# Kernel optimization log

Measured on AMD Instinct MI355X. Metric: run time of the kernel, lower is better.

The kernel has to match this reference:

```python
import jax, jax.numpy as jnp
import numpy as np

B, T, D = 4, 2048, 2048
H = 16
NOPE, ROPE, VD = 64, 64, 128
QK = NOPE + ROPE  # 128
KV_R, Q_R = 512, 1024
EPS = 1e-6
THETA = 10000.0
SCALE = 1.0 / np.sqrt(QK)


def rmsnorm(x, g):
    var = jnp.mean(jnp.square(x), axis=-1, keepdims=True)
    return x * jax.lax.rsqrt(var + EPS) * g


def rope_tables(seq_len, dim):
    inv_freq = 1.0 / (THETA ** (np.arange(0, dim, 2, dtype=np.float32) / dim))
    t = np.arange(seq_len, dtype=np.float32)
    freqs = np.outer(t, inv_freq)              # [T, dim/2]
    emb = np.concatenate([freqs, freqs], -1)   # [T, dim]
    return jnp.asarray(np.cos(emb)), jnp.asarray(np.sin(emb))


def rotate_half(x):
    x1, x2 = jnp.split(x, 2, axis=-1)
    return jnp.concatenate([-x2, x1], axis=-1)


def apply_rope(x, cos, sin):
    # x: [B,H,S,dim]; cos/sin: [S,dim] -> broadcast over B,H
    return x * cos[None, None] + rotate_half(x) * sin[None, None]


def setup_inputs() -> dict:
    key = jax.random.key(0)
    ks = jax.random.split(key, 10)
    w = lambda k, shp: jax.random.normal(k, shp, jnp.float32) * 0.02
    return {
        'x': jax.random.normal(ks[0], (B, T, D), jnp.float32),
        'w_q_down': w(ks[1], (D, Q_R)),
        'g_q_down': jnp.ones((Q_R,), jnp.float32),
        'w_q_up': w(ks[2], (Q_R, H * QK)),
        'w_kv_down': w(ks[3], (D, KV_R)),
        'g_kv_down': jnp.ones((KV_R,), jnp.float32),
        'w_k_up': w(ks[4], (KV_R, H * NOPE)),
        'w_v_up': w(ks[5], (KV_R, H * VD)),
        'w_k_rope': w(ks[6], (D, ROPE)),
        'g_q': jnp.ones((QK,), jnp.float32),
        'g_k': jnp.ones((QK,), jnp.float32),
        'w_gate': w(ks[7], (D, H * VD)),
        'w_o': w(ks[8], (H * VD, D)),
    }


def reference(x, w_q_down, g_q_down, w_q_up, w_kv_down, g_kv_down,
              w_k_up, w_v_up, w_k_rope, g_q, g_k, w_gate, w_o):
    cos, sin = rope_tables(T, ROPE)

    # Low-rank Q: down-proj -> RMSNorm -> up-proj
    q_c = rmsnorm(x @ w_q_down, g_q_down)                       # [B,T,Q_R]
    q = (q_c @ w_q_up).reshape(B, T, H, QK).transpose(0, 2, 1, 3)  # [B,H,T,QK]
    q_nope, q_rope = q[..., :NOPE], q[..., NOPE:]

    # Low-rank KV compression
    c_kv = rmsnorm(x @ w_kv_down, g_kv_down)                    # [B,S,KV_R]
    k_rope = x @ w_k_rope                                       # [B,S,ROPE]
    S = T
    k_nope = (c_kv @ w_k_up).reshape(B, S, H, NOPE).transpose(0, 2, 1, 3)
    v = (c_kv @ w_v_up).reshape(B, S, H, VD).transpose(0, 2, 1, 3)

    # Decoupled RoPE: shared k_rope broadcast over heads
    k_rope = jnp.broadcast_to(k_rope[:, None], (B, H, S, ROPE))
    q_rope = apply_rope(q_rope, cos[:T], sin[:T])
    k_rope = apply_rope(k_rope, cos[:S], sin[:S])

    q = rmsnorm(jnp.concatenate([q_nope, q_rope], -1), g_q)     # [B,H,T,QK]
    k = rmsnorm(jnp.concatenate([k_nope, k_rope], -1), g_k)     # [B,H,S,QK]

    # Causal SDPA
    scores = jnp.einsum('bhtd,bhsd->bhts', q, k) * SCALE
    mask = jnp.tril(jnp.ones((T, S), bool))
    scores = jnp.where(mask, scores, jnp.finfo(scores.dtype).min)
    attn = jax.nn.softmax(scores, axis=-1)
    out = jnp.einsum('bhts,bhsd->bhtd', attn, v)                # [B,H,T,VD]

    # Gating
    gate = (x @ w_gate).reshape(B, T, H, VD).transpose(0, 2, 1, 3)
    out = out * jax.nn.silu(gate)

    out = out.transpose(0, 2, 1, 3).reshape(B, T, H * VD)
    return out @ w_o
```

## Files before the change

kernel.cpp:

```cpp
#include <hip/hip_runtime.h>
#include <hip/hip_bf16.h>
#include <math.h>

typedef __bf16 bf16_t;
typedef __bf16 bf16x8 __attribute__((ext_vector_type(8)));
typedef float f32x4 __attribute__((ext_vector_type(4)));

#define SCALE_F 0.08838834764831845f
#define SMAX_F 14.0f

#define GLOAD_LDS16(gp, lp)                                              \
    __builtin_amdgcn_global_load_lds(                                    \
        (const __attribute__((address_space(1))) void*)(gp),             \
        (__attribute__((address_space(3))) void*)(lp), 16, 0, 0)

__global__ void k_convert(const float* __restrict__ in, bf16_t* __restrict__ out, int n) {
    int i = (blockIdx.x * 256 + threadIdx.x) * 4;
    if (i >= n) return;
    float4 f = *(const float4*)(in + i);
    out[i + 0] = (bf16_t)f.x;
    out[i + 1] = (bf16_t)f.y;
    out[i + 2] = (bf16_t)f.z;
    out[i + 3] = (bf16_t)f.w;
}

__global__ void k_transpose(const float* __restrict__ w, bf16_t* __restrict__ wt, int K, int N) {
    __shared__ float tile[32][33];
    int n0 = blockIdx.x * 32, k0 = blockIdx.y * 32;
    int tx = threadIdx.x & 31, ty = threadIdx.x >> 5;
#pragma unroll
    for (int i = 0; i < 32; i += 8)
        tile[ty + i][tx] = w[(size_t)(k0 + ty + i) * N + (n0 + tx)];
    __syncthreads();
#pragma unroll
    for (int i = 0; i < 32; i += 8)
        wt[(size_t)(n0 + ty + i) * K + (k0 + tx)] = (bf16_t)tile[tx][ty + i];
}

__global__ void k_rope_tables(float* __restrict__ cosT, float* __restrict__ sinT) {
    int idx = blockIdx.x * 256 + threadIdx.x;
    int t = idx >> 6, i = idx & 63;
    float invf = powf(10000.f, -(float)(i & 31) / 32.f);
    float ang = (float)t * invf;
    float s, c;
    sincosf(ang, &s, &c);
    cosT[idx] = c;
    sinT[idx] = s;
}

__global__ void k_rmsnorm(bf16_t* __restrict__ x, const float* __restrict__ g, int C) {
    bf16_t* p = x + (size_t)blockIdx.x * C;
    float ss = 0.f;
    for (int i = threadIdx.x; i < C; i += 256) {
        float v = (float)p[i];
        ss += v * v;
    }
#pragma unroll
    for (int m = 32; m; m >>= 1) ss += __shfl_xor(ss, m);
    __shared__ float red[4];
    if ((threadIdx.x & 63) == 0) red[threadIdx.x >> 6] = ss;
    __syncthreads();
    float tot = red[0] + red[1] + red[2] + red[3];
    float scale = rsqrtf(tot / (float)C + 1e-6f);
    for (int i = threadIdx.x; i < C; i += 256)
        p[i] = (bf16_t)((float)p[i] * scale * g[i]);
}

template <int OUTF32>
__global__ __launch_bounds__(256) void k_gemm(const bf16_t* __restrict__ A,
                                              const bf16_t* __restrict__ Bt,
                                              void* __restrict__ Cp, int M, int N, int K,
                                              size_t sA, size_t sB, size_t sC) {
    __shared__ bf16_t As[128 * 32];
    __shared__ bf16_t Bs[128 * 32];
    A += (size_t)blockIdx.z * sA;
    Bt += (size_t)blockIdx.z * sB;
    const size_t coff = (size_t)blockIdx.z * sC;
    const int bm = blockIdx.y * 128, bn = blockIdx.x * 128;
    const int tid = threadIdx.x, lane = tid & 63, wv = tid >> 6;
    const int quad = lane >> 4, l16 = lane & 15;
    const int wm = (wv >> 1) * 64, wn = (wv & 1) * 64;
    f32x4 acc[4][4] = {};
    const int sr0 = wv * 32 + (lane >> 2);
    const int scc = (lane & 3) * 8;
    bf16_t* ldsA0 = As + (wv * 2) * 512;
    bf16_t* ldsA1 = As + (wv * 2 + 1) * 512;
    bf16_t* ldsB0 = Bs + (wv * 2) * 512;
    bf16_t* ldsB1 = Bs + (wv * 2 + 1) * 512;
    const bool bok0 = (bn + sr0) < N;
    const bool bok1 = (bn + sr0 + 16) < N;
    for (int k0 = 0; k0 < K; k0 += 32) {
        const bf16_t* gA = A + (size_t)(bm + sr0) * K + k0 + scc;
        const bf16_t* gB = Bt + (size_t)(bn + sr0) * K + k0 + scc;
        GLOAD_LDS16(gA, ldsA0);
        GLOAD_LDS16(gA + (size_t)16 * K, ldsA1);
        if (bok0) GLOAD_LDS16(gB, ldsB0);
        if (bok1) GLOAD_LDS16(gB + (size_t)16 * K, ldsB1);
        __syncthreads();
        bf16x8 af[4], bfr[4];
#pragma unroll
        for (int mi = 0; mi < 4; ++mi)
            af[mi] = *(bf16x8*)(As + (wm + mi * 16 + l16) * 32 + quad * 8);
#pragma unroll
        for (int ni = 0; ni < 4; ++ni)
            bfr[ni] = *(bf16x8*)(Bs + (wn + ni * 16 + l16) * 32 + quad * 8);
#pragma unroll
        for (int mi = 0; mi < 4; ++mi)
#pragma unroll
            for (int ni = 0; ni < 4; ++ni)
                acc[mi][ni] =
                    __builtin_amdgcn_mfma_f32_16x16x32_bf16(af[mi], bfr[ni], acc[mi][ni], 0, 0, 0);
        __syncthreads();
    }
#pragma unroll
    for (int mi = 0; mi < 4; ++mi)
#pragma unroll
        for (int ni = 0; ni < 4; ++ni)
#pragma unroll
            for (int r = 0; r < 4; ++r) {
                int row = bm + wm + mi * 16 + quad * 4 + r;
                int col = bn + wn + ni * 16 + l16;
                if (col < N) {
                    if constexpr (OUTF32)
                        ((float*)Cp)[coff + (size_t)row * N + col] = acc[mi][ni][r];
                    else
                        ((bf16_t*)Cp)[coff + (size_t)row * N + col] = (bf16_t)acc[mi][ni][r];
                }
            }
}

__global__ void k_build_q(bf16_t* __restrict__ q, const float* __restrict__ g,
                          const float* __restrict__ cosT, const float* __restrict__ sinT) {
    int wid = blockIdx.x * 4 + (threadIdx.x >> 6);
    int lane = threadIdx.x & 63;
    int row = wid >> 4, h = wid & 15;
    int t = row & 2047;
    bf16_t* p = q + (size_t)row * 2048 + h * 128;
    float x0 = (float)p[lane];
    float x1 = (float)p[64 + lane];
    float xp = (float)p[64 + (lane ^ 32)];
    float c = cosT[t * 64 + lane], s = sinT[t * 64 + lane];
    float rot = (lane < 32) ? -xp : xp;
    float y1 = x1 * c + rot * s;
    float ss = x0 * x0 + y1 * y1;
#pragma unroll
    for (int m = 32; m; m >>= 1) ss += __shfl_xor(ss, m);
    float scale = rsqrtf(ss / 128.f + 1e-6f);
    p[lane] = (bf16_t)(x0 * scale * g[lane]);
    p[64 + lane] = (bf16_t)(y1 * scale * g[64 + lane]);
}

__global__ void k_build_k(const bf16_t* __restrict__ knope, const bf16_t* __restrict__ krope,
                          bf16_t* __restrict__ kout, const float* __restrict__ g,
                          const float* __restrict__ cosT, const float* __restrict__ sinT) {
    int wid = blockIdx.x * 4 + (threadIdx.x >> 6);
    int lane = threadIdx.x & 63;
    int row = wid >> 4, h = wid & 15;
    int t = row & 2047;
    float x0 = (float)knope[(size_t)row * 1024 + h * 64 + lane];
    float x1 = (float)krope[(size_t)row * 64 + lane];
    float xp = (float)krope[(size_t)row * 64 + (lane ^ 32)];
    float c = cosT[t * 64 + lane], s = sinT[t * 64 + lane];
    float rot = (lane < 32) ? -xp : xp;
    float y1 = x1 * c + rot * s;
    float ss = x0 * x0 + y1 * y1;
#pragma unroll
    for (int m = 32; m; m >>= 1) ss += __shfl_xor(ss, m);
    float scale = rsqrtf(ss / 128.f + 1e-6f);
    bf16_t* p = kout + (size_t)row * 2048 + h * 128;
    p[lane] = (bf16_t)(x0 * scale * g[lane]);
    p[64 + lane] = (bf16_t)(y1 * scale * g[64 + lane]);
}

__global__ __launch_bounds__(512, 4) void k_attn(const bf16_t* __restrict__ q,
                                                 const bf16_t* __restrict__ k,
                                                 const bf16_t* __restrict__ vT,
                                                 const bf16_t* __restrict__ gate,
                                                 bf16_t* __restrict__ o) {
    __shared__ bf16_t Ks[64 * 136];
    __shared__ bf16_t Vt[128 * 72];
    __shared__ bf16_t Ps[128 * 72];
    const int qb = (int)gridDim.x - 1 - (int)blockIdx.x;
    const int bh = blockIdx.y;
    const int b = bh >> 4, h = bh & 15;
    const int t0 = qb * 128;
    const int tid = threadIdx.x, lane = tid & 63, wv = tid >> 6;
    const int quad = lane >> 4, l16 = lane & 15;
    const int wrow = t0 + wv * 16;

    bf16x8 aq[4];
    {
        const bf16_t* qp = q + ((size_t)(b * 2048 + wrow + l16)) * 2048 + h * 128 + quad * 8;
#pragma unroll
        for (int kk = 0; kk < 4; ++kk) aq[kk] = *(const bf16x8*)(qp + kk * 32);
    }
    f32x4 oacc[8] = {};
    float l_i[4] = {0.f, 0.f, 0.f, 0.f};

    const bf16_t* vbase = vT + ((size_t)b * 2048 + (size_t)h * 128) * 2048;
    const bf16_t* kbase = k + ((size_t)b * 2048) * 2048 + h * 128;

    const int krow = tid >> 4;
    const int kcol = (tid & 15) * 8;
    const int vrow = tid >> 3;
    const int vcol = (tid & 7) * 8;

    const int nkb = 2 * qb + 2;
    bf16x8 kreg0, kreg1, vreg0, vreg1;
    {
        kreg0 = *(const bf16x8*)(kbase + (size_t)krow * 2048 + kcol);
        kreg1 = *(const bf16x8*)(kbase + (size_t)(krow + 32) * 2048 + kcol);
        vreg0 = *(const bf16x8*)(vbase + (size_t)vrow * 2048 + vcol);
        vreg1 = *(const bf16x8*)(vbase + (size_t)(vrow + 64) * 2048 + vcol);
    }
    for (int kb = 0; kb < nkb; ++kb) {
        const int s0 = kb * 64;
        __syncthreads();
        *(bf16x8*)(Ks + krow * 136 + kcol) = kreg0;
        *(bf16x8*)(Ks + (krow + 32) * 136 + kcol) = kreg1;
        *(bf16x8*)(Vt + vrow * 72 + vcol) = vreg0;
        *(bf16x8*)(Vt + (vrow + 64) * 72 + vcol) = vreg1;
        __syncthreads();
        if (kb + 1 < nkb) {
            const int sn = s0 + 64;
            kreg0 = *(const bf16x8*)(kbase + (size_t)(sn + krow) * 2048 + kcol);
            kreg1 = *(const bf16x8*)(kbase + (size_t)(sn + krow + 32) * 2048 + kcol);
            vreg0 = *(const bf16x8*)(vbase + (size_t)vrow * 2048 + sn + vcol);
            vreg1 = *(const bf16x8*)(vbase + (size_t)(vrow + 64) * 2048 + sn + vcol);
        }
        if (s0 > wrow + 15) continue;
        f32x4 sc[4] = {};
#pragma unroll
        for (int kk = 0; kk < 4; ++kk)
#pragma unroll
            for (int ni = 0; ni < 4; ++ni) {
                bf16x8 bk = *(bf16x8*)(Ks + (ni * 16 + l16) * 136 + kk * 32 + quad * 8);
                sc[ni] = __builtin_amdgcn_mfma_f32_16x16x32_bf16(aq[kk], bk, sc[ni], 0, 0, 0);
            }
        const bool diag = (s0 + 63 > wrow);
        const int trowb = wrow + quad * 4;
#pragma unroll
        for (int ni = 0; ni < 4; ++ni) {
            int scol = s0 + ni * 16 + l16;
#pragma unroll
            for (int r2 = 0; r2 < 4; ++r2) {
                float pv = __expf(sc[ni][r2] * SCALE_F - SMAX_F);
                if (diag && scol > trowb + r2) pv = 0.f;
                sc[ni][r2] = pv;
                l_i[r2] += pv;
            }
        }
#pragma unroll
        for (int ni = 0; ni < 4; ++ni)
#pragma unroll
            for (int r2 = 0; r2 < 4; ++r2)
                Ps[(wv * 16 + quad * 4 + r2) * 72 + ni * 16 + l16] = (bf16_t)sc[ni][r2];
#pragma unroll
        for (int kk = 0; kk < 2; ++kk) {
            bf16x8 ap = *(bf16x8*)(Ps + (wv * 16 + l16) * 72 + kk * 32 + quad * 8);
#pragma unroll
            for (int ni = 0; ni < 8; ++ni) {
                bf16x8 bv = *(bf16x8*)(Vt + (ni * 16 + l16) * 72 + kk * 32 + quad * 8);
                oacc[ni] = __builtin_amdgcn_mfma_f32_16x16x32_bf16(ap, bv, oacc[ni], 0, 0, 0);
            }
        }
    }
#pragma unroll
    for (int m = 8; m; m >>= 1)
#pragma unroll
        for (int r2 = 0; r2 < 4; ++r2) l_i[r2] += __shfl_xor(l_i[r2], m);
    float rl[4];
#pragma unroll
    for (int r2 = 0; r2 < 4; ++r2) rl[r2] = 1.f / l_i[r2];
#pragma unroll
    for (int ni = 0; ni < 8; ++ni) {
        int d = ni * 16 + l16;
#pragma unroll
        for (int r2 = 0; r2 < 4; ++r2) {
            int trow = wrow + quad * 4 + r2;
            size_t gi = ((size_t)(b * 2048 + trow)) * 2048 + h * 128 + d;
            float gt = (float)gate[gi];
            float sg = gt / (1.f + __expf(-gt));
            o[gi] = (bf16_t)((oacc[ni][r2] * rl[r2]) * sg);
        }
    }
}

extern "C" void kernel_launch(void* const* d_in, const int* in_sizes, int n_in,
                              void* d_out, int out_size, void* d_ws, size_t ws_size,
                              hipStream_t stream) {
    const float* x         = (const float*)d_in[0];
    const float* w_q_down  = (const float*)d_in[1];
    const float* g_q_down  = (const float*)d_in[2];
    const float* w_q_up    = (const float*)d_in[3];
    const float* w_kv_down = (const float*)d_in[4];
    const float* g_kv_down = (const float*)d_in[5];
    const float* w_k_up    = (const float*)d_in[6];
    const float* w_v_up    = (const float*)d_in[7];
    const float* w_k_rope  = (const float*)d_in[8];
    const float* g_q       = (const float*)d_in[9];
    const float* g_k       = (const float*)d_in[10];
    const float* w_gate    = (const float*)d_in[11];
    const float* w_o       = (const float*)d_in[12];
    float* out = (float*)d_out;

    char* base = (char*)d_ws;
    size_t off = 0;
    auto alloc = [&](size_t bytes) -> void* {
        void* p = base + off;
        off = (off + bytes + 255) & ~(size_t)255;
        return p;
    };
    const size_t MT = 8192;
    bf16_t* xb     = (bf16_t*)alloc(MT * 2048 * 2);
    bf16_t* wqd_t  = (bf16_t*)alloc((size_t)1024 * 2048 * 2);
    bf16_t* wqu_t  = (bf16_t*)alloc((size_t)2048 * 1024 * 2);
    bf16_t* wkvd_t = (bf16_t*)alloc((size_t)512 * 2048 * 2);
    bf16_t* wku_t  = (bf16_t*)alloc((size_t)1024 * 512 * 2);
    bf16_t* wvu_t  = (bf16_t*)alloc((size_t)2048 * 512 * 2);
    bf16_t* wkr_t  = (bf16_t*)alloc((size_t)64 * 2048 * 2);
    bf16_t* wg_t   = (bf16_t*)alloc((size_t)2048 * 2048 * 2);
    bf16_t* wo_t   = (bf16_t*)alloc((size_t)2048 * 2048 * 2);
    bf16_t* qc     = (bf16_t*)alloc(MT * 1024 * 2);
    bf16_t* ckv    = (bf16_t*)alloc(MT * 512 * 2);
    bf16_t* krope  = (bf16_t*)alloc(MT * 64 * 2);
    bf16_t* vT     = (bf16_t*)alloc(MT * 2048 * 2);
    bf16_t* gbuf   = (bf16_t*)alloc(MT * 2048 * 2);
    float* cosT    = (float*)alloc((size_t)2048 * 64 * 4);
    float* sinT    = (float*)alloc((size_t)2048 * 64 * 4);
    bf16_t* knope = qc;
    bf16_t* qbuf  = (bf16_t*)d_out;
    bf16_t* kbuf  = (bf16_t*)d_out + MT * 2048;
    bf16_t* obuf  = xb;

    k_convert<<<dim3(16384), dim3(256), 0, stream>>>(x, xb, 16777216);
    k_transpose<<<dim3(32, 64), 256, 0, stream>>>(w_q_down, wqd_t, 2048, 1024);
    k_transpose<<<dim3(64, 32), 256, 0, stream>>>(w_q_up, wqu_t, 1024, 2048);
    k_transpose<<<dim3(16, 64), 256, 0, stream>>>(w_kv_down, wkvd_t, 2048, 512);
    k_transpose<<<dim3(32, 16), 256, 0, stream>>>(w_k_up, wku_t, 512, 1024);
    k_transpose<<<dim3(64, 16), 256, 0, stream>>>(w_v_up, wvu_t, 512, 2048);
    k_transpose<<<dim3(2, 64), 256, 0, stream>>>(w_k_rope, wkr_t, 2048, 64);
    k_transpose<<<dim3(64, 64), 256, 0, stream>>>(w_gate, wg_t, 2048, 2048);
    k_transpose<<<dim3(64, 64), 256, 0, stream>>>(w_o, wo_t, 2048, 2048);
    k_rope_tables<<<dim3(512), 256, 0, stream>>>(cosT, sinT);
    k_gemm<0><<<dim3(8, 64), 256, 0, stream>>>(xb, wqd_t, qc, 8192, 1024, 2048, 0, 0, 0);
    k_rmsnorm<<<dim3(8192), 256, 0, stream>>>(qc, g_q_down, 1024);
    k_gemm<0><<<dim3(16, 64), 256, 0, stream>>>(qc, wqu_t, qbuf, 8192, 2048, 1024, 0, 0, 0);
    k_gemm<0><<<dim3(4, 64), 256, 0, stream>>>(xb, wkvd_t, ckv, 8192, 512, 2048, 0, 0, 0);
    k_rmsnorm<<<dim3(8192), 256, 0, stream>>>(ckv, g_kv_down, 512);
    k_gemm<0><<<dim3(8, 64), 256, 0, stream>>>(ckv, wku_t, knope, 8192, 1024, 512, 0, 0, 0);
    k_gemm<0><<<dim3(16, 16, 4), 256, 0, stream>>>(wvu_t, ckv, vT, 2048, 2048, 512,
                                                   0, (size_t)2048 * 512, (size_t)2048 * 2048);
    k_gemm<0><<<dim3(1, 64), 256, 0, stream>>>(xb, wkr_t, krope, 8192, 64, 2048, 0, 0, 0);
    k_gemm<0><<<dim3(16, 64), 256, 0, stream>>>(xb, wg_t, gbuf, 8192, 2048, 2048, 0, 0, 0);
    k_build_q<<<dim3(32768), 256, 0, stream>>>(qbuf, g_q, cosT, sinT);
    k_build_k<<<dim3(32768), 256, 0, stream>>>(knope, krope, kbuf, g_k, cosT, sinT);
    k_attn<<<dim3(16, 64), 512, 0, stream>>>(qbuf, kbuf, vT, gbuf, obuf);
    k_gemm<1><<<dim3(16, 64), 256, 0, stream>>>(obuf, wo_t, out, 8192, 2048, 2048, 0, 0, 0);
}
```

Baseline: 845.1 us.

## Concatenate x-projection weights, fuse rope/norm into q-up GEMM, retile attention

Stacks the four projections that read x (q_down, kv_down, k_rope, gate) into one weight matrix so a single GEMM produces all of them into a wide strided buffer. The two down-projection RMSNorms become one kernel, and the Q up-projection GEMM applies RoPE and the per-head RMSNorm in its epilogue, which removes the separate build_q pass. Attention moves from 512-thread blocks with 16 rows per wave to 256-thread blocks with 32 rows per wave, reusing each K/V fragment across two row sets. Together these cut launches and intermediate round trips, at the cost of more registers per wave in attention and strided reads from the shared buffer.

```diff
diff --git a/kernel.cpp b/kernel.cpp
--- a/kernel.cpp
+++ b/kernel.cpp
@@ -4,10 +4,12 @@
 
 typedef __bf16 bf16_t;
 typedef __bf16 bf16x8 __attribute__((ext_vector_type(8)));
+typedef __bf16 bf16x4v __attribute__((ext_vector_type(4)));
 typedef float f32x4 __attribute__((ext_vector_type(4)));
 
 #define SCALE_F 0.08838834764831845f
 #define SMAX_F 14.0f
+#define OBLD 3712
 
 #define GLOAD_LDS16(gp, lp)                                              \
     __builtin_amdgcn_global_load_lds(                                    \
@@ -37,39 +39,50 @@
         wt[(size_t)(n0 + ty + i) * K + (k0 + tx)] = (bf16_t)tile[tx][ty + i];
 }
 
-__global__ void k_rope_tables(float* __restrict__ cosT, float* __restrict__ sinT) {
+__global__ void k_rope_tables(float2* __restrict__ cs) {
     int idx = blockIdx.x * 256 + threadIdx.x;
     int t = idx >> 6, i = idx & 63;
     float invf = powf(10000.f, -(float)(i & 31) / 32.f);
     float ang = (float)t * invf;
     float s, c;
     sincosf(ang, &s, &c);
-    cosT[idx] = c;
-    sinT[idx] = s;
-}
-
-__global__ void k_rmsnorm(bf16_t* __restrict__ x, const float* __restrict__ g, int C) {
-    bf16_t* p = x + (size_t)blockIdx.x * C;
-    float ss = 0.f;
-    for (int i = threadIdx.x; i < C; i += 256) {
-        float v = (float)p[i];
-        ss += v * v;
-    }
+    cs[idx] = make_float2(c, s);
+}
+
+__global__ void k_rmsnorm2(bf16_t* __restrict__ ob, const float* __restrict__ g1,
+                           const float* __restrict__ g2) {
+    bf16_t* p = ob + (size_t)blockIdx.x * OBLD;
+    const int tid = threadIdx.x;
+    __shared__ float red[4];
+    bf16x4v v = *(bf16x4v*)(p + tid * 4);
+    float a0 = (float)v[0], a1 = (float)v[1], a2 = (float)v[2], a3 = (float)v[3];
+    float ss = a0 * a0 + a1 * a1 + a2 * a2 + a3 * a3;
 #pragma unroll
     for (int m = 32; m; m >>= 1) ss += __shfl_xor(ss, m);
-    __shared__ float red[4];
-    if ((threadIdx.x & 63) == 0) red[threadIdx.x >> 6] = ss;
+    if ((tid & 63) == 0) red[tid >> 6] = ss;
     __syncthreads();
-    float tot = red[0] + red[1] + red[2] + red[3];
-    float scale = rsqrtf(tot / (float)C + 1e-6f);
-    for (int i = threadIdx.x; i < C; i += 256)
-        p[i] = (bf16_t)((float)p[i] * scale * g[i]);
+    float sc1 = rsqrtf((red[0] + red[1] + red[2] + red[3]) / 1024.f + 1e-6f);
+    v[0] = (bf16_t)(a0 * sc1 * g1[tid * 4 + 0]);
+    v[1] = (bf16_t)(a1 * sc1 * g1[tid * 4 + 1]);
+    v[2] = (bf16_t)(a2 * sc1 * g1[tid * 4 + 2]);
+    v[3] = (bf16_t)(a3 * sc1 * g1[tid * 4 + 3]);
+    *(bf16x4v*)(p + tid * 4) = v;
+    float b0 = (float)p[1024 + tid * 2], b1 = (float)p[1024 + tid * 2 + 1];
+    float ss2 = b0 * b0 + b1 * b1;
+#pragma unroll
+    for (int m = 32; m; m >>= 1) ss2 += __shfl_xor(ss2, m);
+    __syncthreads();
+    if ((tid & 63) == 0) red[tid >> 6] = ss2;
+    __syncthreads();
+    float sc2 = rsqrtf((red[0] + red[1] + red[2] + red[3]) / 512.f + 1e-6f);
+    p[1024 + tid * 2] = (bf16_t)(b0 * sc2 * g2[tid * 2]);
+    p[1024 + tid * 2 + 1] = (bf16_t)(b1 * sc2 * g2[tid * 2 + 1]);
 }
 
 template <int OUTF32>
-__global__ __launch_bounds__(256) void k_gemm(const bf16_t* __restrict__ A,
-                                              const bf16_t* __restrict__ Bt,
-                                              void* __restrict__ Cp, int M, int N, int K,
+__global__ __launch_bounds__(256) void k_gemm(const bf16_t* __restrict__ A, int lda,
+                                              const bf16_t* __restrict__ Bt, int ldb,
+                                              void* __restrict__ Cp, int ldc, int M, int N, int K,
                                               size_t sA, size_t sB, size_t sC) {
     __shared__ bf16_t As[128 * 32];
     __shared__ bf16_t Bs[128 * 32];
@@ -90,12 +103,12 @@
     const bool bok0 = (bn + sr0) < N;
     const bool bok1 = (bn + sr0 + 16) < N;
     for (int k0 = 0; k0 < K; k0 += 32) {
-        const bf16_t* gA = A + (size_t)(bm + sr0) * K + k0 + scc;
-        const bf16_t* gB = Bt + (size_t)(bn + sr0) * K + k0 + scc;
+        const bf16_t* gA = A + (size_t)(bm + sr0) * lda + k0 + scc;
+        const bf16_t* gB = Bt + (size_t)(bn + sr0) * ldb + k0 + scc;
         GLOAD_LDS16(gA, ldsA0);
-        GLOAD_LDS16(gA + (size_t)16 * K, ldsA1);
+        GLOAD_LDS16(gA + (size_t)16 * lda, ldsA1);
         if (bok0) GLOAD_LDS16(gB, ldsB0);
-        if (bok1) GLOAD_LDS16(gB + (size_t)16 * K, ldsB1);
+        if (bok1) GLOAD_LDS16(gB + (size_t)16 * ldb, ldsB1);
         __syncthreads();
         bf16x8 af[4], bfr[4];
 #pragma unroll
@@ -122,47 +135,116 @@
                 int col = bn + wn + ni * 16 + l16;
                 if (col < N) {
                     if constexpr (OUTF32)
-                        ((float*)Cp)[coff + (size_t)row * N + col] = acc[mi][ni][r];
+                        ((float*)Cp)[coff + (size_t)row * ldc + col] = acc[mi][ni][r];
                     else
-                        ((bf16_t*)Cp)[coff + (size_t)row * N + col] = (bf16_t)acc[mi][ni][r];
+                        ((bf16_t*)Cp)[coff + (size_t)row * ldc + col] = (bf16_t)acc[mi][ni][r];
                 }
             }
 }
 
-__global__ void k_build_q(bf16_t* __restrict__ q, const float* __restrict__ g,
-                          const float* __restrict__ cosT, const float* __restrict__ sinT) {
-    int wid = blockIdx.x * 4 + (threadIdx.x >> 6);
-    int lane = threadIdx.x & 63;
-    int row = wid >> 4, h = wid & 15;
-    int t = row & 2047;
-    bf16_t* p = q + (size_t)row * 2048 + h * 128;
-    float x0 = (float)p[lane];
-    float x1 = (float)p[64 + lane];
-    float xp = (float)p[64 + (lane ^ 32)];
-    float c = cosT[t * 64 + lane], s = sinT[t * 64 + lane];
-    float rot = (lane < 32) ? -xp : xp;
-    float y1 = x1 * c + rot * s;
-    float ss = x0 * x0 + y1 * y1;
-#pragma unroll
-    for (int m = 32; m; m >>= 1) ss += __shfl_xor(ss, m);
-    float scale = rsqrtf(ss / 128.f + 1e-6f);
-    p[lane] = (bf16_t)(x0 * scale * g[lane]);
-    p[64 + lane] = (bf16_t)(y1 * scale * g[64 + lane]);
+__global__ __launch_bounds__(256) void k_gemm_qup(const bf16_t* __restrict__ A, int lda,
+                                                  const bf16_t* __restrict__ Bt,
+                                                  bf16_t* __restrict__ Cq,
+                                                  const float* __restrict__ g_q,
+                                                  const float2* __restrict__ cs, int K) {
+    __shared__ bf16_t As[128 * 32];
+    __shared__ bf16_t Bs[128 * 32];
+    __shared__ float red[2][128];
+    const int ldb = K;
+    const int bm = blockIdx.y * 128, bn = blockIdx.x * 128;
+    const int h = blockIdx.x;
+    const int tid = threadIdx.x, lane = tid & 63, wv = tid >> 6;
+    const int quad = lane >> 4, l16 = lane & 15;
+    const int wm = (wv >> 1) * 64, wn = (wv & 1) * 64;
+    f32x4 acc[4][4] = {};
+    const int sr0 = wv * 32 + (lane >> 2);
+    const int scc = (lane & 3) * 8;
+    bf16_t* ldsA0 = As + (wv * 2) * 512;
+    bf16_t* ldsA1 = As + (wv * 2 + 1) * 512;
+    bf16_t* ldsB0 = Bs + (wv * 2) * 512;
+    bf16_t* ldsB1 = Bs + (wv * 2 + 1) * 512;
+    for (int k0 = 0; k0 < K; k0 += 32) {
+        const bf16_t* gA = A + (size_t)(bm + sr0) * lda + k0 + scc;
+        const bf16_t* gB = Bt + (size_t)(bn + sr0) * ldb + k0 + scc;
+        GLOAD_LDS16(gA, ldsA0);
+        GLOAD_LDS16(gA + (size_t)16 * lda, ldsA1);
+        GLOAD_LDS16(gB, ldsB0);
+        GLOAD_LDS16(gB + (size_t)16 * ldb, ldsB1);
+        __syncthreads();
+        bf16x8 af[4], bfr[4];
+#pragma unroll
+        for (int mi = 0; mi < 4; ++mi)
+            af[mi] = *(bf16x8*)(As + (wm + mi * 16 + l16) * 32 + quad * 8);
+#pragma unroll
+        for (int ni = 0; ni < 4; ++ni)
+            bfr[ni] = *(bf16x8*)(Bs + (wn + ni * 16 + l16) * 32 + quad * 8);
+#pragma unroll
+        for (int mi = 0; mi < 4; ++mi)
+#pragma unroll
+            for (int ni = 0; ni < 4; ++ni)
+                acc[mi][ni] =
+                    __builtin_amdgcn_mfma_f32_16x16x32_bf16(af[mi], bfr[ni], acc[mi][ni], 0, 0, 0);
+        __syncthreads();
+    }
+    if (wn) {
+#pragma unroll
+        for (int mi = 0; mi < 4; ++mi)
+#pragma unroll
+            for (int r = 0; r < 4; ++r) {
+                int t = (bm + wm + mi * 16 + quad * 4 + r) & 2047;
+                float2 c0 = cs[t * 64 + 0 * 16 + l16];
+                float2 c1 = cs[t * 64 + 1 * 16 + l16];
+                float2 c2 = cs[t * 64 + 2 * 16 + l16];
+                float2 c3 = cs[t * 64 + 3 * 16 + l16];
+                float a0 = acc[mi][0][r], a1 = acc[mi][1][r];
+                float a2 = acc[mi][2][r], a3 = acc[mi][3][r];
+                acc[mi][0][r] = a0 * c0.x - a2 * c0.y;
+                acc[mi][1][r] = a1 * c1.x - a3 * c1.y;
+                acc[mi][2][r] = a2 * c2.x + a0 * c2.y;
+                acc[mi][3][r] = a3 * c3.x + a1 * c3.y;
+            }
+    }
+#pragma unroll
+    for (int mi = 0; mi < 4; ++mi)
+#pragma unroll
+        for (int r = 0; r < 4; ++r) {
+            float ss = acc[mi][0][r] * acc[mi][0][r] + acc[mi][1][r] * acc[mi][1][r] +
+                       acc[mi][2][r] * acc[mi][2][r] + acc[mi][3][r] * acc[mi][3][r];
+#pragma unroll
+            for (int m = 8; m; m >>= 1) ss += __shfl_xor(ss, m);
+            if (l16 == 0) red[wn >> 6][wm + mi * 16 + quad * 4 + r] = ss;
+        }
+    __syncthreads();
+    float gv[4];
+#pragma unroll
+    for (int ni = 0; ni < 4; ++ni) gv[ni] = g_q[wn + ni * 16 + l16];
+#pragma unroll
+    for (int mi = 0; mi < 4; ++mi)
+#pragma unroll
+        for (int r = 0; r < 4; ++r) {
+            int row = wm + mi * 16 + quad * 4 + r;
+            float tot = red[0][row] + red[1][row];
+            float scale = rsqrtf(tot / 128.f + 1e-6f);
+            size_t gi = (size_t)(bm + row) * 2048 + h * 128 + wn + l16;
+#pragma unroll
+            for (int ni = 0; ni < 4; ++ni)
+                Cq[gi + ni * 16] = (bf16_t)(acc[mi][ni][r] * scale * gv[ni]);
+        }
 }
 
 __global__ void k_build_k(const bf16_t* __restrict__ knope, const bf16_t* __restrict__ krope,
                           bf16_t* __restrict__ kout, const float* __restrict__ g,
-                          const float* __restrict__ cosT, const float* __restrict__ sinT) {
+                          const float2* __restrict__ cs) {
     int wid = blockIdx.x * 4 + (threadIdx.x >> 6);
     int lane = threadIdx.x & 63;
     int row = wid >> 4, h = wid & 15;
     int t = row & 2047;
     float x0 = (float)knope[(size_t)row * 1024 + h * 64 + lane];
-    float x1 = (float)krope[(size_t)row * 64 + lane];
-    float xp = (float)krope[(size_t)row * 64 + (lane ^ 32)];
-    float c = cosT[t * 64 + lane], s = sinT[t * 64 + lane];
+    float x1 = (float)krope[(size_t)row * OBLD + lane];
+    float xp = (float)krope[(size_t)row * OBLD + (lane ^ 32)];
+    float2 c = cs[t * 64 + lane];
     float rot = (lane < 32) ? -xp : xp;
-    float y1 = x1 * c + rot * s;
+    float y1 = x1 * c.x + rot * c.y;
     float ss = x0 * x0 + y1 * y1;
 #pragma unroll
     for (int m = 32; m; m >>= 1) ss += __shfl_xor(ss, m);
@@ -172,11 +254,11 @@
     p[64 + lane] = (bf16_t)(y1 * scale * g[64 + lane]);
 }
 
-__global__ __launch_bounds__(512, 4) void k_attn(const bf16_t* __restrict__ q,
-                                                 const bf16_t* __restrict__ k,
-                                                 const bf16_t* __restrict__ vT,
-                                                 const bf16_t* __restrict__ gate,
-                                                 bf16_t* __restrict__ o) {
+__global__ __launch_bounds__(256) void k_attn(const bf16_t* __restrict__ q,
+                                              const bf16_t* __restrict__ k,
+                                              const bf16_t* __restrict__ vT,
+                                              const bf16_t* __restrict__ gate,
+                                              bf16_t* __restrict__ o) {
     __shared__ bf16_t Ks[64 * 136];
     __shared__ bf16_t Vt[128 * 72];
     __shared__ bf16_t Ps[128 * 72];
@@ -186,102 +268,114 @@
     const int t0 = qb * 128;
     const int tid = threadIdx.x, lane = tid & 63, wv = tid >> 6;
     const int quad = lane >> 4, l16 = lane & 15;
-    const int wrow = t0 + wv * 16;
-
-    bf16x8 aq[4];
-    {
-        const bf16_t* qp = q + ((size_t)(b * 2048 + wrow + l16)) * 2048 + h * 128 + quad * 8;
-#pragma unroll
-        for (int kk = 0; kk < 4; ++kk) aq[kk] = *(const bf16x8*)(qp + kk * 32);
-    }
-    f32x4 oacc[8] = {};
-    float l_i[4] = {0.f, 0.f, 0.f, 0.f};
-
+    const int wrow = t0 + wv * 32;
+
+    bf16x8 aq[2][4];
+#pragma unroll
+    for (int s = 0; s < 2; ++s) {
+        const bf16_t* qp =
+            q + ((size_t)(b * 2048 + wrow + s * 16 + l16)) * 2048 + h * 128 + quad * 8;
+#pragma unroll
+        for (int kk = 0; kk < 4; ++kk) aq[s][kk] = *(const bf16x8*)(qp + kk * 32);
+    }
+    f32x4 oacc[2][8] = {};
+    float l_i[2][4] = {};
+
+    const bf16_t* kbase = k + ((size_t)b * 2048) * 2048 + h * 128;
     const bf16_t* vbase = vT + ((size_t)b * 2048 + (size_t)h * 128) * 2048;
-    const bf16_t* kbase = k + ((size_t)b * 2048) * 2048 + h * 128;
-
-    const int krow = tid >> 4;
-    const int kcol = (tid & 15) * 8;
-    const int vrow = tid >> 3;
-    const int vcol = (tid & 7) * 8;
+
+    const int krow = tid >> 4, kcol = (tid & 15) * 8;
+    const int vrow = tid >> 3, vcol = (tid & 7) * 8;
 
     const int nkb = 2 * qb + 2;
-    bf16x8 kreg0, kreg1, vreg0, vreg1;
-    {
-        kreg0 = *(const bf16x8*)(kbase + (size_t)krow * 2048 + kcol);
-        kreg1 = *(const bf16x8*)(kbase + (size_t)(krow + 32) * 2048 + kcol);
-        vreg0 = *(const bf16x8*)(vbase + (size_t)vrow * 2048 + vcol);
-        vreg1 = *(const bf16x8*)(vbase + (size_t)(vrow + 64) * 2048 + vcol);
+    bf16x8 kreg[4], vreg[4];
+#pragma unroll
+    for (int p = 0; p < 4; ++p) {
+        kreg[p] = *(const bf16x8*)(kbase + (size_t)(krow + p * 16) * 2048 + kcol);
+        vreg[p] = *(const bf16x8*)(vbase + (size_t)(vrow + p * 32) * 2048 + vcol);
     }
     for (int kb = 0; kb < nkb; ++kb) {
         const int s0 = kb * 64;
         __syncthreads();
-        *(bf16x8*)(Ks + krow * 136 + kcol) = kreg0;
-        *(bf16x8*)(Ks + (krow + 32) * 136 + kcol) = kreg1;
-        *(bf16x8*)(Vt + vrow * 72 + vcol) = vreg0;
-        *(bf16x8*)(Vt + (vrow + 64) * 72 + vcol) = vreg1;
+#pragma unroll
+        for (int p = 0; p < 4; ++p) {
+            *(bf16x8*)(Ks + (krow + p * 16) * 136 + kcol) = kreg[p];
+            *(bf16x8*)(Vt + (vrow + p * 32) * 72 + vcol) = vreg[p];
+        }
         __syncthreads();
         if (kb + 1 < nkb) {
             const int sn = s0 + 64;
-            kreg0 = *(const bf16x8*)(kbase + (size_t)(sn + krow) * 2048 + kcol);
-            kreg1 = *(const bf16x8*)(kbase + (size_t)(sn + krow + 32) * 2048 + kcol);
-            vreg0 = *(const bf16x8*)(vbase + (size_t)vrow * 2048 + sn + vcol);
-            vreg1 = *(const bf16x8*)(vbase + (size_t)(vrow + 64) * 2048 + sn + vcol);
-        }
-        if (s0 > wrow + 15) continue;
-        f32x4 sc[4] = {};
+#pragma unroll
+            for (int p = 0; p < 4; ++p) {
+                kreg[p] = *(const bf16x8*)(kbase + (size_t)(sn + krow + p * 16) * 2048 + kcol);
+                vreg[p] = *(const bf16x8*)(vbase + (size_t)(vrow + p * 32) * 2048 + sn + vcol);
+            }
+        }
+        if (s0 > wrow + 31) continue;
+        f32x4 sc[2][4] = {};
 #pragma unroll
         for (int kk = 0; kk < 4; ++kk)
 #pragma unroll
             for (int ni = 0; ni < 4; ++ni) {
                 bf16x8 bk = *(bf16x8*)(Ks + (ni * 16 + l16) * 136 + kk * 32 + quad * 8);
-                sc[ni] = __builtin_amdgcn_mfma_f32_16x16x32_bf16(aq[kk], bk, sc[ni], 0, 0, 0);
-            }
-        const bool diag = (s0 + 63 > wrow);
-        const int trowb = wrow + quad * 4;
-#pragma unroll
-        for (int ni = 0; ni < 4; ++ni) {
-            int scol = s0 + ni * 16 + l16;
-#pragma unroll
-            for (int r2 = 0; r2 < 4; ++r2) {
-                float pv = __expf(sc[ni][r2] * SCALE_F - SMAX_F);
-                if (diag && scol > trowb + r2) pv = 0.f;
-                sc[ni][r2] = pv;
-                l_i[r2] += pv;
-            }
-        }
-#pragma unroll
-        for (int ni = 0; ni < 4; ++ni)
-#pragma unroll
-            for (int r2 = 0; r2 < 4; ++r2)
-                Ps[(wv * 16 + quad * 4 + r2) * 72 + ni * 16 + l16] = (bf16_t)sc[ni][r2];
+                sc[0][ni] = __builtin_amdgcn_mfma_f32_16x16x32_bf16(aq[0][kk], bk, sc[0][ni], 0, 0, 0);
+                sc[1][ni] = __builtin_amdgcn_mfma_f32_16x16x32_bf16(aq[1][kk], bk, sc[1][ni], 0, 0, 0);
+            }
+#pragma unroll
+        for (int s = 0; s < 2; ++s) {
+            const int trowb = wrow + s * 16 + quad * 4;
+            const bool diag = (s0 + 63 > trowb + 3) | true;
+#pragma unroll
+            for (int ni = 0; ni < 4; ++ni) {
+                int scol = s0 + ni * 16 + l16;
+#pragma unroll
+                for (int r2 = 0; r2 < 4; ++r2) {
+                    float pv = __expf(sc[s][ni][r2] * SCALE_F - SMAX_F);
+                    if (scol > trowb + r2) pv = 0.f;
+                    sc[s][ni][r2] = pv;
+                    l_i[s][r2] += pv;
+                }
+            }
+            (void)diag;
+#pragma unroll
+            for (int ni = 0; ni < 4; ++ni)
+#pragma unroll
+                for (int r2 = 0; r2 < 4; ++r2)
+                    Ps[(wv * 32 + s * 16 + quad * 4 + r2) * 72 + ni * 16 + l16] =
+                        (bf16_t)sc[s][ni][r2];
+        }
 #pragma unroll
         for (int kk = 0; kk < 2; ++kk) {
-            bf16x8 ap = *(bf16x8*)(Ps + (wv * 16 + l16) * 72 + kk * 32 + quad * 8);
+            bf16x8 ap0 = *(bf16x8*)(Ps + (wv * 32 + l16) * 72 + kk * 32 + quad * 8);
+            bf16x8 ap1 = *(bf16x8*)(Ps + (wv * 32 + 16 + l16) * 72 + kk * 32 + quad * 8);
 #pragma unroll
             for (int ni = 0; ni < 8; ++ni) {
                 bf16x8 bv = *(bf16x8*)(Vt + (ni * 16 + l16) * 72 + kk * 32 + quad * 8);
-                oacc[ni] = __builtin_amdgcn_mfma_f32_16x16x32_bf16(ap, bv, oacc[ni], 0, 0, 0);
-            }
-        }
-    }
-#pragma unroll
-    for (int m = 8; m; m >>= 1)
-#pragma unroll
-        for (int r2 = 0; r2 < 4; ++r2) l_i[r2] += __shfl_xor(l_i[r2], m);
-    float rl[4];
-#pragma unroll
-    for (int r2 = 0; r2 < 4; ++r2) rl[r2] = 1.f / l_i[r2];
-#pragma unroll
-    for (int ni = 0; ni < 8; ++ni) {
-        int d = ni * 16 + l16;
-#pragma unroll
-        for (int r2 = 0; r2 < 4; ++r2) {
-            int trow = wrow + quad * 4 + r2;
-            size_t gi = ((size_t)(b * 2048 + trow)) * 2048 + h * 128 + d;
-            float gt = (float)gate[gi];
-            float sg = gt / (1.f + __expf(-gt));
-            o[gi] = (bf16_t)((oacc[ni][r2] * rl[r2]) * sg);
+                oacc[0][ni] = __builtin_amdgcn_mfma_f32_16x16x32_bf16(ap0, bv, oacc[0][ni], 0, 0, 0);
+                oacc[1][ni] = __builtin_amdgcn_mfma_f32_16x16x32_bf16(ap1, bv, oacc[1][ni], 0, 0, 0);
+            }
+        }
+    }
+#pragma unroll
+    for (int s = 0; s < 2; ++s) {
+#pragma unroll
+        for (int m = 8; m; m >>= 1)
+#pragma unroll
+            for (int r2 = 0; r2 < 4; ++r2) l_i[s][r2] += __shfl_xor(l_i[s][r2], m);
+        float rl[4];
+#pragma unroll
+        for (int r2 = 0; r2 < 4; ++r2) rl[r2] = 1.f / l_i[s][r2];
+#pragma unroll
+        for (int ni = 0; ni < 8; ++ni) {
+            int d = ni * 16 + l16;
+#pragma unroll
+            for (int r2 = 0; r2 < 4; ++r2) {
+                int trow = wrow + s * 16 + quad * 4 + r2;
+                size_t grow = (size_t)(b * 2048 + trow);
+                float gt = (float)gate[grow * OBLD + 1600 + h * 128 + d];
+                float sg = gt / (1.f + __expf(-gt));
+                o[grow * 2048 + h * 128 + d] = (bf16_t)((oacc[s][ni][r2] * rl[r2]) * sg);
+            }
         }
     }
 }
@@ -312,49 +406,41 @@
         return p;
     };
     const size_t MT = 8192;
-    bf16_t* xb     = (bf16_t*)alloc(MT * 2048 * 2);
-    bf16_t* wqd_t  = (bf16_t*)alloc((size_t)1024 * 2048 * 2);
-    bf16_t* wqu_t  = (bf16_t*)alloc((size_t)2048 * 1024 * 2);
-    bf16_t* wkvd_t = (bf16_t*)alloc((size_t)512 * 2048 * 2);
-    bf16_t* wku_t  = (bf16_t*)alloc((size_t)1024 * 512 * 2);
-    bf16_t* wvu_t  = (bf16_t*)alloc((size_t)2048 * 512 * 2);
-    bf16_t* wkr_t  = (bf16_t*)alloc((size_t)64 * 2048 * 2);
-    bf16_t* wg_t   = (bf16_t*)alloc((size_t)2048 * 2048 * 2);
-    bf16_t* wo_t   = (bf16_t*)alloc((size_t)2048 * 2048 * 2);
-    bf16_t* qc     = (bf16_t*)alloc(MT * 1024 * 2);
-    bf16_t* ckv    = (bf16_t*)alloc(MT * 512 * 2);
-    bf16_t* krope  = (bf16_t*)alloc(MT * 64 * 2);
-    bf16_t* vT     = (bf16_t*)alloc(MT * 2048 * 2);
-    bf16_t* gbuf   = (bf16_t*)alloc(MT * 2048 * 2);
-    float* cosT    = (float*)alloc((size_t)2048 * 64 * 4);
-    float* sinT    = (float*)alloc((size_t)2048 * 64 * 4);
-    bf16_t* knope = qc;
+    bf16_t* xb    = (bf16_t*)alloc(MT * 2048 * 2);
+    bf16_t* Wt    = (bf16_t*)alloc((size_t)OBLD * 2048 * 2);
+    bf16_t* wqu_t = (bf16_t*)alloc((size_t)2048 * 1024 * 2);
+    bf16_t* wku_t = (bf16_t*)alloc((size_t)1024 * 512 * 2);
+    bf16_t* wvu_t = (bf16_t*)alloc((size_t)2048 * 512 * 2);
+    bf16_t* wo_t  = (bf16_t*)alloc((size_t)2048 * 2048 * 2);
+    bf16_t* ob    = (bf16_t*)alloc(MT * OBLD * 2);
+    bf16_t* knope = (bf16_t*)alloc(MT * 1024 * 2);
+    bf16_t* vT    = (bf16_t*)alloc(MT * 2048 * 2);
+    float2* cs    = (float2*)alloc((size_t)2048 * 64 * 8);
     bf16_t* qbuf  = (bf16_t*)d_out;
     bf16_t* kbuf  = (bf16_t*)d_out + MT * 2048;
     bf16_t* obuf  = xb;
 
     k_convert<<<dim3(16384), dim3(256), 0, stream>>>(x, xb, 16777216);
-    k_transpose<<<dim3(32, 64), 256, 0, stream>>>(w_q_down, wqd_t, 2048, 1024);
+    k_rope_tables<<<dim3(512), 256, 0, stream>>>(cs);
+    k_transpose<<<dim3(32, 64), 256, 0, stream>>>(w_q_down, Wt, 2048, 1024);
+    k_transpose<<<dim3(16, 64), 256, 0, stream>>>(w_kv_down, Wt + (size_t)1024 * 2048, 2048, 512);
+    k_transpose<<<dim3(2, 64), 256, 0, stream>>>(w_k_rope, Wt + (size_t)1536 * 2048, 2048, 64);
+    k_transpose<<<dim3(64, 64), 256, 0, stream>>>(w_gate, Wt + (size_t)1600 * 2048, 2048, 2048);
     k_transpose<<<dim3(64, 32), 256, 0, stream>>>(w_q_up, wqu_t, 1024, 2048);
-    k_transpose<<<dim3(16, 64), 256, 0, stream>>>(w_kv_down, wkvd_t, 2048, 512);
     k_transpose<<<dim3(32, 16), 256, 0, stream>>>(w_k_up, wku_t, 512, 1024);
     k_transpose<<<dim3(64, 16), 256, 0, stream>>>(w_v_up, wvu_t, 512, 2048);
-    k_transpose<<<dim3(2, 64), 256, 0, stream>>>(w_k_rope, wkr_t, 2048, 64);
-    k_transpose<<<dim3(64, 64), 256, 0, stream>>>(w_gate, wg_t, 2048, 2048);
     k_transpose<<<dim3(64, 64), 256, 0, stream>>>(w_o, wo_t, 2048, 2048);
-    k_rope_tables<<<dim3(512), 256, 0, stream>>>(cosT, sinT);
-    k_gemm<0><<<dim3(8, 64), 256, 0, stream>>>(xb, wqd_t, qc, 8192, 1024, 2048, 0, 0, 0);
-    k_rmsnorm<<<dim3(8192), 256, 0, stream>>>(qc, g_q_down, 1024);
-    k_gemm<0><<<dim3(16, 64), 256, 0, stream>>>(qc, wqu_t, qbuf, 8192, 2048, 1024, 0, 0, 0);
-    k_gemm<0><<<dim3(4, 64), 256, 0, stream>>>(xb, wkvd_t, ckv, 8192, 512, 2048, 0, 0, 0);
-    k_rmsnorm<<<dim3(8192), 256, 0, stream>>>(ckv, g_kv_down, 512);
-    k_gemm<0><<<dim3(8, 64), 256, 0, stream>>>(ckv, wku_t, knope, 8192, 1024, 512, 0, 0, 0);
-    k_gemm<0><<<dim3(16, 16, 4), 256, 0, stream>>>(wvu_t, ckv, vT, 2048, 2048, 512,
-                                                   0, (size_t)2048 * 512, (size_t)2048 * 2048);
-    k_gemm<0><<<dim3(1, 64), 256, 0, stream>>>(xb, wkr_t, krope, 8192, 64, 2048, 0, 0, 0);
-    k_gemm<0><<<dim3(16, 64), 256, 0, stream>>>(xb, wg_t, gbuf, 8192, 2048, 2048, 0, 0, 0);
-    k_build_q<<<dim3(32768), 256, 0, stream>>>(qbuf, g_q, cosT, sinT);
-    k_build_k<<<dim3(32768), 256, 0, stream>>>(knope, krope, kbuf, g_k, cosT, sinT);
-    k_attn<<<dim3(16, 64), 512, 0, stream>>>(qbuf, kbuf, vT, gbuf, obuf);
-    k_gemm<1><<<dim3(16, 64), 256, 0, stream>>>(obuf, wo_t, out, 8192, 2048, 2048, 0, 0, 0);
-}
+    k_gemm<0><<<dim3(29, 64), 256, 0, stream>>>(xb, 2048, Wt, 2048, ob, OBLD, 8192, 3648, 2048,
+                                                0, 0, 0);
+    k_rmsnorm2<<<dim3(8192), 256, 0, stream>>>(ob, g_q_down, g_kv_down);
+    k_gemm_qup<<<dim3(16, 64), 256, 0, stream>>>(ob, OBLD, wqu_t, qbuf, g_q, cs, 1024);
+    k_gemm<0><<<dim3(8, 64), 256, 0, stream>>>(ob + 1024, OBLD, wku_t, 512, knope, 1024,
+                                               8192, 1024, 512, 0, 0, 0);
+    k_gemm<0><<<dim3(16, 16, 4), 256, 0, stream>>>(wvu_t, 512, ob + 1024, OBLD, vT, 2048,
+                                                   2048, 2048, 512, 0, (size_t)2048 * OBLD,
+                                                   (size_t)2048 * 2048);
+    k_build_k<<<dim3(32768), 256, 0, stream>>>(knope, ob + 1536, kbuf, g_k, cs);
+    k_attn<<<dim3(16, 64), 256, 0, stream>>>(qbuf, kbuf, vT, ob, obuf);
+    k_gemm<1><<<dim3(16, 64), 256, 0, stream>>>(obuf, 2048, wo_t, 2048, out, 2048,
+                                                8192, 2048, 2048, 0, 0, 0);
+}
```

Result: slower. 907.5 us (+7.4%).
